# Kernel optimization log

Measured on AMD Instinct MI355X. Metric: run time of the kernel, lower is better.

Reference implementation:

```python
import jax, jax.numpy as jnp
import numpy as np

N, F, E, B, D = 100000, 256, 128, 10000, 32
GAMMA, ZETA = -0.1, 1.1  # hard-concrete stretch params of L0Dense


def setup_inputs() -> dict:
    key = jax.random.key(0)
    ks = jax.random.split(key, 12)
    return {
        "nodes": jax.random.randint(ks[0], (B,), 0, N),
        "neigh_idx": jax.random.randint(ks[1], (B, D), 0, N),
        "neigh_mask": jax.random.bernoulli(ks[2], 0.9, (B, D)),
        "feature": jax.random.normal(ks[3], (N, F), jnp.float32),
        "W": jax.random.normal(ks[4], (F, E), jnp.float32) * 0.05,
        "b": jnp.zeros((E,), jnp.float32),
        "qz_loga": jax.random.normal(ks[5], (F,), jnp.float32),
        "att1_w": jax.random.normal(ks[6], (2 * E, E), jnp.float32) * 0.05,
        "att1_b": jnp.zeros((E,), jnp.float32),
        "att2_w": jax.random.normal(ks[7], (E, E), jnp.float32) * 0.05,
        "att2_b": jnp.zeros((E,), jnp.float32),
        "att3_w": jax.random.normal(ks[8], (E, 1), jnp.float32) * 0.05,
        "att3_b": jnp.zeros((1,), jnp.float32),
    }


def reference(nodes, neigh_idx, neigh_mask, feature, W, b, qz_loga,
              att1_w, att1_b, att2_w, att2_b, att3_w, att3_b):
    # L0Dense, deterministic (eval) hard-concrete gate on input dims
    z = jnp.clip(jax.nn.sigmoid(qz_loga) * (ZETA - GAMMA) + GAMMA, 0.0, 1.0)
    We = W * z[:, None]                                  # [F, E]

    node_feat = feature[nodes] @ We + b                   # [B, E]
    neigh_feat = feature[neigh_idx] @ We + b              # [B, D, E]

    # GraphRec-style attention MLP over (neighbor, center) pairs
    h = jnp.concatenate(
        [neigh_feat, jnp.broadcast_to(node_feat[:, None, :], neigh_feat.shape)],
        axis=-1)                                          # [B, D, 2E]
    h = jax.nn.relu(h @ att1_w + att1_b)
    h = jax.nn.relu(h @ att2_w + att2_b)
    scores = (h @ att3_w + att3_b)[..., 0]                # [B, D]
    scores = jnp.where(neigh_mask, scores, -1e30)
    att = jax.nn.softmax(scores, axis=-1)                 # [B, D]

    agg = jnp.einsum('bd,bde->be', att, neigh_feat)       # weighted sum
    has_neigh = neigh_mask.any(axis=-1, keepdims=True)
    return jnp.where(has_neigh, agg, node_feat)           # n==0 fallback
```

## Files before the change

kernel.cpp:

```cpp
#include <hip/hip_runtime.h>
#include <hip/hip_bf16.h>
#include <math.h>

#define NN 100000
#define FF 256
#define EE 128
#define BB_ 10000
#define DD 32

typedef __attribute__((ext_vector_type(8))) short short8;
typedef __attribute__((ext_vector_type(4))) float f32x4;

__device__ __forceinline__ short f2bf(float f) {
  __hip_bfloat16 h = __float2bfloat16(f);
  union { __hip_bfloat16 h; short s; } u; u.h = h;
  return u.s;
}
__device__ __forceinline__ float bf2f(short s) {
  union { unsigned u; float f; } v;
  v.u = ((unsigned)(unsigned short)s) << 16;
  return v.f;
}

__device__ __forceinline__ void gll16(const float* g, float* lds) {
  __builtin_amdgcn_global_load_lds(
      (const __attribute__((address_space(1))) unsigned int*)g,
      (__attribute__((address_space(3))) unsigned int*)lds, 16, 0, 0);
}

__global__ __launch_bounds__(256) void k_prep(
    const float* __restrict__ W, const float* __restrict__ qz,
    const float* __restrict__ a1w, const float* __restrict__ a2w,
    const float* __restrict__ bb,
    float* __restrict__ Wef32, short* __restrict__ BT2,
    short* __restrict__ a1wTc, short* __restrict__ w2T,
    float* __restrict__ bias2) {
  int i = blockIdx.x * 256 + threadIdx.x;
  if (i < 32768) {
    int f = i >> 7, e = i & 127;
    float g = qz[f];
    float s = 1.0f / (1.0f + expf(-g));
    float z = fminf(fmaxf(s * 1.2f - 0.1f, 0.0f), 1.0f);
    float v = W[f * 128 + e] * z;
    Wef32[f * 128 + e] = v;
    BT2[e * 256 + f] = f2bf(v);
  } else if (i < 49152) {
    int t = i - 32768; int n = t >> 7, k = t & 127;
    a1wTc[n * 128 + k] = f2bf(a1w[(128 + k) * 128 + n]);
  } else if (i < 65536) {
    int t = i - 49152; int n = t >> 7, k = t & 127;
    w2T[n * 128 + k] = f2bf(a2w[k * 128 + n]);
  } else if (i < 65664) {
    bias2[i - 65536] = bb[i - 65536];
  }
}

__global__ __launch_bounds__(256) void k_compose(
    const float* __restrict__ Wef32, const float* __restrict__ a1w,
    const float* __restrict__ a1b, const float* __restrict__ bb,
    short* __restrict__ BT2, float* __restrict__ bias2) {
  const int n = blockIdx.x;
  const int f = threadIdx.x;
  float s = 0.f;
  for (int e = 0; e < 128; ++e)
    s = fmaf(a1w[e * 128 + n], Wef32[f * 128 + e], s);
  BT2[(size_t)(128 + n) * 256 + f] = f2bf(s);
  if (f == 0) {
    float by = a1b[n];
    for (int e = 0; e < 128; ++e) by = fmaf(bb[e], a1w[e * 128 + n], by);
    bias2[128 + n] = by;
  }
}

__global__ __launch_bounds__(256, 2) void k_xy(
    const float* __restrict__ feat, const short* __restrict__ BT2,
    const float* __restrict__ bias2, short* __restrict__ XY, int M) {
  __shared__ float As[64 * 256];
  const int tid = threadIdx.x;
  const int mb = blockIdx.x * 64;
  const int wave = tid >> 6, lane = tid & 63;
  const int wn = wave;
  const int l15 = lane & 15, lg = lane >> 4;

#pragma unroll
  for (int it = 0; it < 16; ++it) {
    int r = it * 4 + wave;
    int grow = mb + r;
    if (grow >= M) grow = M - 1;
    gll16(feat + (size_t)grow * 256 + ((lane ^ (r & 7)) * 4), As + r * 256);
  }

  short8 bfr[8][4];
#pragma unroll
  for (int ks = 0; ks < 8; ++ks)
#pragma unroll
    for (int j = 0; j < 4; ++j)
      bfr[ks][j] = *(const short8*)(BT2 +
          (size_t)(wn * 64 + j * 16 + l15) * 256 + (ks * 4 + lg) * 8);

  __syncthreads();

  f32x4 acc[4][4];
#pragma unroll
  for (int i = 0; i < 4; ++i)
#pragma unroll
    for (int j = 0; j < 4; ++j) acc[i][j] = (f32x4){0.f, 0.f, 0.f, 0.f};

#pragma unroll
  for (int ks = 0; ks < 8; ++ks) {
    const int kg = ks * 4 + lg;
#pragma unroll
    for (int i = 0; i < 4; ++i) {
      const int r = i * 16 + l15;
      const int sw = r & 7;
      const int c0 = (2 * kg) ^ sw;
      const int c1 = (2 * kg + 1) ^ sw;
      float4 flo = *(const float4*)(As + r * 256 + c0 * 4);
      float4 fhi = *(const float4*)(As + r * 256 + c1 * 4);
      short8 af;
      af[0] = f2bf(flo.x); af[1] = f2bf(flo.y);
      af[2] = f2bf(flo.z); af[3] = f2bf(flo.w);
      af[4] = f2bf(fhi.x); af[5] = f2bf(fhi.y);
      af[6] = f2bf(fhi.z); af[7] = f2bf(fhi.w);
      __builtin_amdgcn_s_setprio(1);
#pragma unroll
      for (int j = 0; j < 4; ++j)
        acc[i][j] = __builtin_amdgcn_mfma_f32_16x16x32_bf16(
            af, bfr[ks][j], acc[i][j], 0, 0, 0);
      __builtin_amdgcn_s_setprio(0);
    }
  }

  float bv4[4];
#pragma unroll
  for (int j = 0; j < 4; ++j) bv4[j] = bias2[wn * 64 + j * 16 + l15];
#pragma unroll
  for (int i = 0; i < 4; ++i) {
#pragma unroll
    for (int r = 0; r < 4; ++r) {
      int row = mb + i * 16 + lg * 4 + r;
      if (row < M) {
#pragma unroll
        for (int j = 0; j < 4; ++j) {
          int col = wn * 64 + j * 16 + l15;
          XY[(size_t)row * 256 + col] = f2bf(acc[i][j][r] + bv4[j]);
        }
      }
    }
  }
}

template <int K, int LDA, int LDC, bool AF32, bool OUTBF16>
__global__ __launch_bounds__(256) void k_mm(
    const void* __restrict__ Ap, const short* __restrict__ BT,
    const float* __restrict__ bias, const int* __restrict__ idx,
    void* __restrict__ Cp, int M) {
  __shared__ short As[128 * 64];
  __shared__ short Bs[128 * 64];
  const int tid = threadIdx.x;
  const int mb = blockIdx.x * 128;
  const int col0 = blockIdx.y * 128;
  const int wave = tid >> 6, lane = tid & 63;
  const int wr = wave >> 1, wc = wave & 1;
  const int l15 = lane & 15, lg = lane >> 4;

  size_t abase[4];
#pragma unroll
  for (int s = 0; s < 4; ++s) {
    int row = (tid + s * 256) >> 3;
    int grow = mb + row;
    int gr = 0;
    if (grow < M) gr = idx ? idx[grow] : grow;
    abase[s] = (size_t)gr * LDA;
  }

  f32x4 acc[4][4];
#pragma unroll
  for (int i = 0; i < 4; ++i)
#pragma unroll
    for (int j = 0; j < 4; ++j) acc[i][j] = (f32x4){0.f, 0.f, 0.f, 0.f};

  for (int k0 = 0; k0 < K; k0 += 64) {
#pragma unroll
    for (int s = 0; s < 4; ++s) {
      int q = tid + s * 256;
      int row = q >> 3, c = q & 7;
      short8 av;
      if (AF32) {
        const float* ap = (const float*)Ap + abase[s] + k0 + c * 8;
        float4 f0 = *(const float4*)ap;
        float4 f1 = *(const float4*)(ap + 4);
        av[0] = f2bf(f0.x); av[1] = f2bf(f0.y);
        av[2] = f2bf(f0.z); av[3] = f2bf(f0.w);
        av[4] = f2bf(f1.x); av[5] = f2bf(f1.y);
        av[6] = f2bf(f1.z); av[7] = f2bf(f1.w);
      } else {
        av = *(const short8*)((const short*)Ap + abase[s] + k0 + c * 8);
      }
      *(short8*)(As + row * 64 + 8 * (c ^ (row & 7))) = av;
      short8 bv = *(const short8*)(BT + (size_t)(col0 + row) * K + k0 + c * 8);
      *(short8*)(Bs + row * 64 + 8 * (c ^ (row & 7))) = bv;
    }
    __syncthreads();
#pragma unroll
    for (int ks = 0; ks < 2; ++ks) {
      int c = ks * 4 + lg;
      short8 af[4], bfv[4];
#pragma unroll
      for (int i = 0; i < 4; ++i) {
        int r = wr * 64 + i * 16 + l15;
        af[i] = *(short8*)(As + r * 64 + 8 * (c ^ (r & 7)));
        int n = wc * 64 + i * 16 + l15;
        bfv[i] = *(short8*)(Bs + n * 64 + 8 * (c ^ (n & 7)));
      }
#pragma unroll
      for (int i = 0; i < 4; ++i)
#pragma unroll
        for (int j = 0; j < 4; ++j)
          acc[i][j] = __builtin_amdgcn_mfma_f32_16x16x32_bf16(
              af[i], bfv[j], acc[i][j], 0, 0, 0);
    }
    __syncthreads();
  }

  float bv4[4];
#pragma unroll
  for (int j = 0; j < 4; ++j) {
    int col = wc * 64 + j * 16 + l15;
    bv4[j] = bias ? bias[col0 + col] : 0.f;
  }
#pragma unroll
  for (int i = 0; i < 4; ++i) {
#pragma unroll
    for (int r = 0; r < 4; ++r) {
      int row = mb + wr * 64 + i * 16 + lg * 4 + r;
      if (row < M) {
#pragma unroll
        for (int j = 0; j < 4; ++j) {
          int col = wc * 64 + j * 16 + l15;
          float v = acc[i][j][r] + bv4[j];
          if (OUTBF16)
            ((short*)Cp)[(size_t)row * LDC + col0 + col] = f2bf(v);
          else
            ((float*)Cp)[(size_t)row * LDC + col0 + col] = v;
        }
      }
    }
  }
}

__global__ __launch_bounds__(256) void k_attn4(
    const short* __restrict__ XY, const float* __restrict__ P,
    const int* __restrict__ nodes, const int* __restrict__ nidx,
    const int* __restrict__ nmask, const short* __restrict__ w2T,
    const float* __restrict__ b2, const float* __restrict__ w3,
    const float* __restrict__ b3, float* __restrict__ out) {
  __shared__ int ni_s[4][32];
  __shared__ float sc_s[4][32];
  __shared__ float att_s[4][32];
  const int tid = threadIdx.x;
  const int wave = tid >> 6, lane = tid & 63;
  const int b = blockIdx.x * 4 + wave;
  const int l15 = lane & 15, lg = lane >> 4;

  if (lane < 32) ni_s[wave][lane] = nidx[b * DD + lane];

  const int m = nmask[(size_t)b * DD + (lane & 31)];
  const int nid0 = ni_s[wave][l15];
  const int nid1 = ni_s[wave][16 + l15];
  const short* yr0 = XY + (size_t)nid0 * 256 + 128;
  const short* yr1 = XY + (size_t)nid1 * 256 + 128;
  short8 y0v[4], y1v[4];
#pragma unroll
  for (int ks = 0; ks < 4; ++ks) {
    const int k0 = ks * 32 + lg * 8;
    y0v[ks] = *(const short8*)(yr0 + k0);
    y1v[ks] = *(const short8*)(yr1 + k0);
  }
  unsigned xv[32];
#pragma unroll
  for (int d = 0; d < 32; ++d)
    xv[d] = *(const unsigned*)(XY + (size_t)ni_s[wave][d] * 256 + 2 * lane);

  const float* pr = P + (size_t)b * EE;

  f32x4 acc[2][8];
#pragma unroll
  for (int i = 0; i < 2; ++i)
#pragma unroll
    for (int j = 0; j < 8; ++j) acc[i][j] = (f32x4){0.f, 0.f, 0.f, 0.f};

#pragma unroll
  for (int ks = 0; ks < 4; ++ks) {
    const int k0 = ks * 32 + lg * 8;
    float4 pa = *(const float4*)(pr + k0);
    float4 pb = *(const float4*)(pr + k0 + 4);
    float pf[8] = {pa.x, pa.y, pa.z, pa.w, pb.x, pb.y, pb.z, pb.w};
    short8 a0, a1;
#pragma unroll
    for (int e = 0; e < 8; ++e) {
      a0[e] = f2bf(fmaxf(bf2f(y0v[ks][e]) + pf[e], 0.f));
      a1[e] = f2bf(fmaxf(bf2f(y1v[ks][e]) + pf[e], 0.f));
    }
    short8 bfv[8];
#pragma unroll
    for (int j = 0; j < 8; ++j)
      bfv[j] = *(const short8*)(w2T + (size_t)(j * 16 + l15) * EE + k0);
    __builtin_amdgcn_s_setprio(1);
#pragma unroll
    for (int j = 0; j < 8; ++j) {
      acc[0][j] = __builtin_amdgcn_mfma_f32_16x16x32_bf16(a0, bfv[j],
                                                          acc[0][j], 0, 0, 0);
      acc[1][j] = __builtin_amdgcn_mfma_f32_16x16x32_bf16(a1, bfv[j],
                                                          acc[1][j], 0, 0, 0);
    }
    __builtin_amdgcn_s_setprio(0);
  }

  float b2v[8], w3v[8];
#pragma unroll
  for (int j = 0; j < 8; ++j) {
    int col = j * 16 + l15;
    b2v[j] = b2[col];
    w3v[j] = w3[col];
  }
  float part[2][4];
#pragma unroll
  for (int i = 0; i < 2; ++i)
#pragma unroll
    for (int r = 0; r < 4; ++r) {
      float s = 0.f;
#pragma unroll
      for (int j = 0; j < 8; ++j)
        s += fmaxf(acc[i][j][r] + b2v[j], 0.f) * w3v[j];
      part[i][r] = s;
    }
#pragma unroll
  for (int off = 1; off <= 8; off <<= 1) {
#pragma unroll
    for (int i = 0; i < 2; ++i)
#pragma unroll
      for (int r = 0; r < 4; ++r) part[i][r] += __shfl_xor(part[i][r], off);
  }
  if (l15 == 0) {
#pragma unroll
    for (int i = 0; i < 2; ++i)
#pragma unroll
      for (int r = 0; r < 4; ++r)
        sc_s[wave][i * 16 + lg * 4 + r] = part[i][r];
  }

  const int row = lane & 31;
  float s = sc_s[wave][row] + b3[0];
  if (!m) s = -1e30f;
  float mx = s;
#pragma unroll
  for (int off = 1; off <= 16; off <<= 1) mx = fmaxf(mx, __shfl_xor(mx, off));
  float e = expf(s - mx);
  float sum = e;
#pragma unroll
  for (int off = 1; off <= 16; off <<= 1) sum += __shfl_xor(sum, off);
  if (lane < 32) att_s[wave][row] = e / sum;
  const bool has = (__ballot(m != 0) != 0ull);

  float a0 = 0.f, a1 = 0.f;
  if (has) {
#pragma unroll
    for (int d = 0; d < 32; ++d) {
      float a = att_s[wave][d];
      a0 += a * bf2f((short)(xv[d] & 0xffffu));
      a1 += a * bf2f((short)(xv[d] >> 16));
    }
  } else {
    const short* xr = XY + (size_t)nodes[b] * 256;
    unsigned x2 = *(const unsigned*)(xr + 2 * lane);
    a0 = bf2f((short)(x2 & 0xffffu));
    a1 = bf2f((short)(x2 >> 16));
  }
  *(float2*)(out + (size_t)b * EE + 2 * lane) = make_float2(a0, a1);
}

extern "C" void kernel_launch(void* const* d_in, const int* in_sizes, int n_in,
                              void* d_out, int out_size, void* d_ws,
                              size_t ws_size, hipStream_t stream) {
  const int* nodes = (const int*)d_in[0];
  const int* nidx = (const int*)d_in[1];
  const int* nmask = (const int*)d_in[2];
  const float* feature = (const float*)d_in[3];
  const float* W = (const float*)d_in[4];
  const float* bb = (const float*)d_in[5];
  const float* qz = (const float*)d_in[6];
  const float* a1w = (const float*)d_in[7];
  const float* a1b = (const float*)d_in[8];
  const float* a2w = (const float*)d_in[9];
  const float* a2b = (const float*)d_in[10];
  const float* a3w = (const float*)d_in[11];
  const float* a3b = (const float*)d_in[12];
  float* out = (float*)d_out;

  char* ws = (char*)d_ws;
  short* BT2   = (short*)(ws);
  float* Wef32 = (float*)(ws + 131072);
  short* a1wTc = (short*)(ws + 262144);
  short* w2T   = (short*)(ws + 294912);
  float* bias2 = (float*)(ws + 327680);
  short* XYb   = (short*)(ws + 524288);
  float* Pv    = (float*)(ws + 524288 + 51200000);

  k_prep<<<257, 256, 0, stream>>>(W, qz, a1w, a2w, bb, Wef32, BT2, a1wTc, w2T,
                                  bias2);
  k_compose<<<128, 256, 0, stream>>>(Wef32, a1w, a1b, bb, BT2, bias2);
  k_xy<<<(NN + 63) / 64, 256, 0, stream>>>(feature, BT2, bias2, XYb, NN);
  k_mm<128, 256, 128, false, false><<<dim3((BB_ + 127) / 128, 1), 256, 0,
                                      stream>>>(XYb, a1wTc, nullptr, nodes, Pv,
                                                BB_);
  k_attn4<<<BB_ / 4, 256, 0, stream>>>(XYb, Pv, nodes, nidx, nmask, w2T, a2b,
                                       a3w, a3b, out);
}
```

Measured before the change: 141.6 us.

## Make k_xy persistent with double-buffered async LDS loads of feature tiles

Converts the feature-projection GEMM into a persistent kernel with 512 blocks, each looping over 32-row tiles. The next tile is prefetched into a second LDS buffer with async global-to-LDS loads while the current tile is processed, and the B fragments are loaded into registers only once per block. This targets the exposed load latency and the repeated B-fragment loads of the one-tile-per-block design. In exchange it relies on manual vmcnt waits and assumes M is a multiple of 32, which holds for NN=100000, so there is no tail handling.

```diff
diff --git a/kernel.cpp b/kernel.cpp
--- a/kernel.cpp
+++ b/kernel.cpp
@@ -72,23 +72,16 @@
   }
 }
 
-__global__ __launch_bounds__(256, 2) void k_xy(
+__global__ __launch_bounds__(256) void k_xy(
     const float* __restrict__ feat, const short* __restrict__ BT2,
     const float* __restrict__ bias2, short* __restrict__ XY, int M) {
-  __shared__ float As[64 * 256];
+  __shared__ float As[2][32 * 256];
   const int tid = threadIdx.x;
-  const int mb = blockIdx.x * 64;
   const int wave = tid >> 6, lane = tid & 63;
   const int wn = wave;
   const int l15 = lane & 15, lg = lane >> 4;
-
-#pragma unroll
-  for (int it = 0; it < 16; ++it) {
-    int r = it * 4 + wave;
-    int grow = mb + r;
-    if (grow >= M) grow = M - 1;
-    gll16(feat + (size_t)grow * 256 + ((lane ^ (r & 7)) * 4), As + r * 256);
-  }
+  const int NT = M >> 5;
+  const int G = gridDim.x;
 
   short8 bfr[8][4];
 #pragma unroll
@@ -97,49 +90,75 @@
     for (int j = 0; j < 4; ++j)
       bfr[ks][j] = *(const short8*)(BT2 +
           (size_t)(wn * 64 + j * 16 + l15) * 256 + (ks * 4 + lg) * 8);
-
-  __syncthreads();
-
-  f32x4 acc[4][4];
-#pragma unroll
-  for (int i = 0; i < 4; ++i)
-#pragma unroll
-    for (int j = 0; j < 4; ++j) acc[i][j] = (f32x4){0.f, 0.f, 0.f, 0.f};
-
-#pragma unroll
-  for (int ks = 0; ks < 8; ++ks) {
-    const int kg = ks * 4 + lg;
-#pragma unroll
-    for (int i = 0; i < 4; ++i) {
-      const int r = i * 16 + l15;
-      const int sw = r & 7;
-      const int c0 = (2 * kg) ^ sw;
-      const int c1 = (2 * kg + 1) ^ sw;
-      float4 flo = *(const float4*)(As + r * 256 + c0 * 4);
-      float4 fhi = *(const float4*)(As + r * 256 + c1 * 4);
-      short8 af;
-      af[0] = f2bf(flo.x); af[1] = f2bf(flo.y);
-      af[2] = f2bf(flo.z); af[3] = f2bf(flo.w);
-      af[4] = f2bf(fhi.x); af[5] = f2bf(fhi.y);
-      af[6] = f2bf(fhi.z); af[7] = f2bf(fhi.w);
-      __builtin_amdgcn_s_setprio(1);
-#pragma unroll
-      for (int j = 0; j < 4; ++j)
-        acc[i][j] = __builtin_amdgcn_mfma_f32_16x16x32_bf16(
-            af, bfr[ks][j], acc[i][j], 0, 0, 0);
-      __builtin_amdgcn_s_setprio(0);
-    }
-  }
-
   float bv4[4];
 #pragma unroll
   for (int j = 0; j < 4; ++j) bv4[j] = bias2[wn * 64 + j * 16 + l15];
-#pragma unroll
-  for (int i = 0; i < 4; ++i) {
-#pragma unroll
-    for (int r = 0; r < 4; ++r) {
-      int row = mb + i * 16 + lg * 4 + r;
-      if (row < M) {
+
+  int t = blockIdx.x;
+  if (t < NT) {
+#pragma unroll
+    for (int it = 0; it < 8; ++it) {
+      int r = it * 4 + wave;
+      gll16(feat + (size_t)(t * 32 + r) * 256 + ((lane ^ (r & 7)) * 4),
+            &As[0][r * 256]);
+    }
+  }
+
+  int cur = 0;
+  for (; t < NT; t += G) {
+    const int tn = t + G;
+    __builtin_amdgcn_s_barrier();
+    if (tn < NT) {
+#pragma unroll
+      for (int it = 0; it < 8; ++it) {
+        int r = it * 4 + wave;
+        gll16(feat + (size_t)(tn * 32 + r) * 256 + ((lane ^ (r & 7)) * 4),
+              &As[cur ^ 1][r * 256]);
+      }
+      asm volatile("s_waitcnt vmcnt(8)" ::: "memory");
+    } else {
+      asm volatile("s_waitcnt vmcnt(0)" ::: "memory");
+    }
+    __builtin_amdgcn_s_barrier();
+    __builtin_amdgcn_sched_barrier(0);
+
+    f32x4 acc[2][4];
+#pragma unroll
+    for (int i = 0; i < 2; ++i)
+#pragma unroll
+      for (int j = 0; j < 4; ++j) acc[i][j] = (f32x4){0.f, 0.f, 0.f, 0.f};
+
+    const float* Ab = &As[cur][0];
+#pragma unroll
+    for (int ks = 0; ks < 8; ++ks) {
+      const int kg = ks * 4 + lg;
+#pragma unroll
+      for (int i = 0; i < 2; ++i) {
+        const int r = i * 16 + l15;
+        const int sw = r & 7;
+        const int c0 = (2 * kg) ^ sw;
+        const int c1 = (2 * kg + 1) ^ sw;
+        float4 flo = *(const float4*)(Ab + r * 256 + c0 * 4);
+        float4 fhi = *(const float4*)(Ab + r * 256 + c1 * 4);
+        short8 af;
+        af[0] = f2bf(flo.x); af[1] = f2bf(flo.y);
+        af[2] = f2bf(flo.z); af[3] = f2bf(flo.w);
+        af[4] = f2bf(fhi.x); af[5] = f2bf(fhi.y);
+        af[6] = f2bf(fhi.z); af[7] = f2bf(fhi.w);
+        __builtin_amdgcn_s_setprio(1);
+#pragma unroll
+        for (int j = 0; j < 4; ++j)
+          acc[i][j] = __builtin_amdgcn_mfma_f32_16x16x32_bf16(
+              af, bfr[ks][j], acc[i][j], 0, 0, 0);
+        __builtin_amdgcn_s_setprio(0);
+      }
+    }
+
+#pragma unroll
+    for (int i = 0; i < 2; ++i) {
+#pragma unroll
+      for (int r = 0; r < 4; ++r) {
+        int row = t * 32 + i * 16 + lg * 4 + r;
 #pragma unroll
         for (int j = 0; j < 4; ++j) {
           int col = wn * 64 + j * 16 + l15;
@@ -147,6 +166,7 @@
         }
       }
     }
+    cur ^= 1;
   }
 }
 
@@ -410,7 +430,7 @@
   k_prep<<<257, 256, 0, stream>>>(W, qz, a1w, a2w, bb, Wef32, BT2, a1wTc, w2T,
                                   bias2);
   k_compose<<<128, 256, 0, stream>>>(Wef32, a1w, a1b, bb, BT2, bias2);
-  k_xy<<<(NN + 63) / 64, 256, 0, stream>>>(feature, BT2, bias2, XYb, NN);
+  k_xy<<<512, 256, 0, stream>>>(feature, BT2, bias2, XYb, NN);
   k_mm<128, 256, 128, false, false><<<dim3((BB_ + 127) / 128, 1), 256, 0,
                                       stream>>>(XYb, a1wTc, nullptr, nodes, Pv,
                                                 BB_);
```

New measurement: 117.9 us. 16.7% less time.
